# Kernel optimization log

Measured on AMD Instinct MI355X. Metric: run time of the kernel, lower is better.

The kernel has to match this reference:

```python
import math
import jax, jax.numpy as jnp
import numpy as np

B, T, FDIM, ODIM = 16, 16, 64, 8
NQ, LAYERS, DEGREE = 10, 2, 3
NA = 4                      # ceil(log2(T))
TOT = NQ + NA               # 14 total wires
NROTS = 4 * NQ * LAYERS     # 80 params per timestep
QROTS = 4 * NQ              # 40 (qff circuit, 1 layer)
C64 = jnp.complex64


def ry_mat(t):
    c = jnp.cos(0.5 * t).astype(C64)
    s = jnp.sin(0.5 * t).astype(C64)
    return jnp.stack([jnp.stack([c, -s], -1), jnp.stack([s, c], -1)], -2)


def rz_mat(t):
    p = jnp.exp(-0.5j * t.astype(C64))
    q = jnp.exp(0.5j * t.astype(C64))
    z = jnp.zeros_like(p)
    return jnp.stack([jnp.stack([p, z], -1), jnp.stack([z, q], -1)], -2)


def crx_mat(t):
    c = jnp.cos(0.5 * t).astype(C64)
    s = (-1j) * jnp.sin(0.5 * t).astype(C64)
    z = jnp.zeros_like(c)
    o = jnp.ones_like(c)
    r0 = jnp.stack([o, z, z, z], -1)
    r1 = jnp.stack([z, o, z, z], -1)
    r2 = jnp.stack([z, z, c, s], -1)
    r3 = jnp.stack([z, z, s, c], -1)
    return jnp.stack([r0, r1, r2, r3], -2)


CNOT = jnp.array([[1, 0, 0, 0], [0, 1, 0, 0], [0, 0, 0, 1], [0, 0, 1, 0]], dtype=C64)


def apply_gate(state, U, wires):
    # state: (Be, 2,...,2) tensor; wire w lives on axis w+1. U: (2^k,2^k) or (Be,2^k,2^k)
    k = len(wires)
    axes = [w + 1 for w in wires]
    st = jnp.moveaxis(state, axes, list(range(1, k + 1)))
    shp = st.shape
    st = st.reshape(shp[0], 2 ** k, -1)
    eq = 'bij,bjr->bir' if U.ndim == 3 else 'ij,bjr->bir'
    st = jnp.einsum(eq, U, st).reshape(shp)
    return jnp.moveaxis(st, list(range(1, k + 1)), axes)


def sim14_seq(nq, layers):
    # gate sequence of Sim et al. circuit 14: RY ring, CRX ring, RY ring, CRX counter-ring
    seq, idx = [], 0
    for _ in range(layers):
        for i in range(nq):
            seq.append(('ry', (i,), idx)); idx += 1
        for i in range(nq - 1, -1, -1):
            seq.append(('crx', (i, (i + 1) % nq), idx)); idx += 1
        for i in range(nq):
            seq.append(('ry', (i,), idx)); idx += 1
        for i in [nq - 1] + list(range(nq - 1)):
            seq.append(('crx', (i, (i - 1) % nq), idx)); idx += 1
    return seq


def apply_sim14(state, params, layers, adjoint=False):
    seq = sim14_seq(NQ, layers)
    if adjoint:
        seq = seq[::-1]
    sign = -1.0 if adjoint else 1.0
    for kind, w, pidx in seq:
        th = sign * params[..., pidx]
        U = ry_mat(th) if kind == 'ry' else crx_mat(th)
        state = apply_gate(state, U, list(w))
    return state


def apply_prepare(state, prep_p, adjoint=False):
    # learnable PREPARE ansatz on ancilla wires NQ..NQ+NA-1 (n_prep_layers == NA)
    seq = []
    for ly in range(NA):
        for qi in range(NA):
            seq.append(('ry', NQ + qi, (ly, qi, 0)))
            seq.append(('rz', NQ + qi, (ly, qi, 1)))
        for i in range(NA - 1):
            seq.append(('cnot', (NQ + i, NQ + i + 1), None))
    if adjoint:
        seq = seq[::-1]
    sign = -1.0 if adjoint else 1.0
    for kind, w, pix in seq:
        if kind == 'cnot':
            state = apply_gate(state, CNOT, list(w))
        else:
            th = sign * prep_p[pix]
            U = ry_mat(th) if kind == 'ry' else rz_mat(th)
            state = apply_gate(state, U, [w])
    return state


def pcphase(state, phi):
    # PennyLane PCPhase(phi, dim=2^NQ, wires=anc+main): e^{+i phi} on ancilla==0 subspace, e^{-i phi} elsewhere
    st = state.reshape(B, 2 ** NQ, 2 ** NA)
    ph = jnp.exp(1j * phi.astype(C64))
    vec = jnp.where(jnp.arange(2 ** NA) == 0, ph, jnp.conj(ph))
    return (st * vec).reshape((B,) + (2,) * TOT)


def apply_select(state, ts_params, adjoint=False):
    # Select: apply sim14(ts_params[:, j]) on main wires when ancilla register == j
    # (T == 2^NA so there is no identity padding). Vectorized over batch x ancilla index.
    st = state.reshape(B, 2 ** NQ, 2 ** NA)
    st = jnp.moveaxis(st, 2, 1).reshape((B * T,) + (2,) * NQ)
    st = apply_sim14(st, ts_params.reshape(B * T, NROTS), LAYERS, adjoint)
    st = st.reshape(B, 2 ** NA, 2 ** NQ)
    return jnp.moveaxis(st, 1, 2).reshape((B,) + (2,) * TOT)


def expvals(state):
    # <X_i>, <Y_i>, <Z_i> on main wires, order X0..X9, Y0..Y9, Z0..Z9
    xs, ys, zs = [], [], []
    for i in range(NQ):
        s = jnp.moveaxis(state, i + 1, 1).reshape(B, 2, -1)
        s0, s1 = s[:, 0], s[:, 1]
        c = jnp.sum(jnp.conj(s0) * s1, axis=-1)
        xs.append(2.0 * jnp.real(c))
        ys.append(2.0 * jnp.imag(c))
        zs.append(jnp.sum(jnp.abs(s0) ** 2 - jnp.abs(s1) ** 2, axis=-1))
    return jnp.stack(xs + ys + zs, axis=1).astype(jnp.float32)  # (B, 3*NQ)


def make_pe():
    pos = np.arange(T, dtype=np.float32)[:, None]
    div = np.exp(np.arange(0, FDIM, 2, dtype=np.float32) * -(math.log(10000.0) / FDIM))
    pe = np.zeros((T, FDIM), np.float32)
    pe[:, 0::2] = np.sin(pos * div)
    pe[:, 1::2] = np.cos(pos * div[:FDIM // 2])
    return jnp.asarray(pe)


def setup_inputs():
    key = jax.random.key(0)
    ks = jax.random.split(key, 8)
    return {
        'x': jax.random.normal(ks[0], (B, FDIM, T), jnp.float32),
        'W_fp': jax.random.normal(ks[1], (NROTS, FDIM), jnp.float32) / math.sqrt(FDIM),
        'b_fp': jnp.zeros((NROTS,), jnp.float32),
        'prep_p': 0.1 * jax.random.normal(ks[2], (NA, NA, 2), jnp.float32),
        'sig_ang': 0.1 * jax.random.normal(ks[3], (DEGREE + 1,), jnp.float32),
        'qff_p': jax.random.uniform(ks[4], (QROTS,), jnp.float32),
        'W_out': jax.random.normal(ks[5], (ODIM, 3 * NQ), jnp.float32) / math.sqrt(3 * NQ),
        'b_out': jnp.zeros((ODIM,), jnp.float32),
    }


def reference(x, W_fp, b_fp, prep_p, sig_ang, qff_p, W_out, b_out):
    h = jnp.transpose(x, (0, 2, 1)) + make_pe()[None]          # (B, T, FDIM)
    ts = jax.nn.sigmoid(h @ W_fp.T + b_fp) * (2.0 * math.pi)    # (B, T, NROTS)
    # |0...0> on all 14 wires, batched
    psi = jnp.zeros((B, 2 ** TOT), C64).at[:, 0].set(1.0).reshape((B,) + (2,) * TOT)
    psi = pcphase(psi, sig_ang[0])
    for k in range(DEGREE):
        psi = apply_prepare(psi, prep_p, adjoint=False)
        psi = apply_select(psi, ts, adjoint=(k % 2 == 1))
        psi = apply_prepare(psi, prep_p, adjoint=True)
        psi = pcphase(psi, sig_ang[k + 1])
    psi = apply_sim14(psi, qff_p, layers=1, adjoint=False)      # QFF readout circuit
    exps = expvals(psi)                                         # (B, 30)
    return exps @ W_out.T + b_out                               # (B, ODIM)
```

## Files before the change

kernel.cpp:

```cpp
#include <hip/hip_runtime.h>
#include <math.h>
#include <utility>


typedef float v2f __attribute__((ext_vector_type(2)));

struct Gate { int ry; int tbit; int cbit; int pidx; };
struct GateTab { Gate g[40]; };

constexpr GateTab make_gates1() {
  GateTab tb{};
  int pos = 0, idx = 0;
  for (int i = 0; i < 10; ++i) { tb.g[pos] = Gate{1, 9 - i, -1, idx}; ++pos; ++idx; }
  for (int i = 9; i >= 0; --i) { tb.g[pos] = Gate{0, 9 - ((i + 1) % 10), 9 - i, idx}; ++pos; ++idx; }
  for (int i = 0; i < 10; ++i) { tb.g[pos] = Gate{1, 9 - i, -1, idx}; ++pos; ++idx; }
  for (int k = 0; k < 10; ++k) {
    int i = (k == 0) ? 9 : (k - 1);
    tb.g[pos] = Gate{0, 9 - ((i + 9) % 10), 9 - i, idx}; ++pos; ++idx;
  }
  return tb;
}
constexpr GateTab GTC = make_gates1();

__device__ __forceinline__ int insert_zero(int v, int p) {
  return ((v >> p) << (p + 1)) | (v & ((1 << p) - 1));
}
__device__ __forceinline__ float2 cmul(float2 A, float2 B) {
  return make_float2(A.x * B.x - A.y * B.y, A.x * B.y + A.y * B.x);
}
__device__ __forceinline__ float2 conj2(float2 A) { return make_float2(A.x, -A.y); }
__device__ __forceinline__ v2f vmk(float x, float y) { v2f r; r.x = x; r.y = y; return r; }

template<int XM>
__device__ __forceinline__ float lxor(float v) {
  if constexpr (XM == 1) {
    int r = __builtin_amdgcn_update_dpp(__float_as_int(v), __float_as_int(v),
                                        0xB1, 0xF, 0xF, true);
    return __int_as_float(r);
  } else if constexpr (XM == 2) {
    int r = __builtin_amdgcn_update_dpp(__float_as_int(v), __float_as_int(v),
                                        0x4E, 0xF, 0xF, true);
    return __int_as_float(r);
  } else if constexpr (XM == 4) {
    int r = __builtin_amdgcn_ds_swizzle(__float_as_int(v), 0x101F);
    return __int_as_float(r);
  } else if constexpr (XM == 8) {
    int r = __builtin_amdgcn_update_dpp(__float_as_int(v), __float_as_int(v),
                                        0x128, 0xF, 0xF, true);
    return __int_as_float(r);
  } else if constexpr (XM == 16) {
#if __has_builtin(__builtin_amdgcn_permlane16_swap)
    unsigned uv = __float_as_uint(v);
    auto r = __builtin_amdgcn_permlane16_swap(uv, uv, false, false);
    return __uint_as_float(r[0] ^ r[1] ^ uv);
#else
    return __shfl_xor(v, 16, 64);
#endif
  } else {
#if __has_builtin(__builtin_amdgcn_permlane32_swap)
    unsigned uv = __float_as_uint(v);
    auto r = __builtin_amdgcn_permlane32_swap(uv, uv, false, false);
    return __uint_as_float(r[0] ^ r[1] ^ uv);
#else
    return __shfl_xor(v, 32, 64);
#endif
  }
}
template<int XM>
__device__ __forceinline__ v2f lxor2(v2f v) {
  v2f r; r.x = lxor<XM>(v.x); r.y = lxor<XM>(v.y); return r;
}

__device__ __forceinline__ float wave_sum(float v) {
  v += lxor<1>(v);
  v += lxor<2>(v);
  v += lxor<4>(v);
  v += lxor<8>(v);
  v += lxor<16>(v);
  v += lxor<32>(v);
  return v;
}

struct alignas(256) GBar {
  unsigned cnt;
  unsigned gen;
  unsigned done;
  unsigned pad[61];
};
__device__ GBar g_gb[16];

__device__ __forceinline__ void group_barrier16(int b, int lane) {
  unsigned snap = __hip_atomic_load(&g_gb[b].gen, __ATOMIC_RELAXED, __HIP_MEMORY_SCOPE_AGENT);
  if (lane == 0) {
    unsigned old = __hip_atomic_fetch_add(&g_gb[b].cnt, 1u, __ATOMIC_ACQ_REL,
                                          __HIP_MEMORY_SCOPE_AGENT);
    if ((old & 15u) == 15u)
      __hip_atomic_store(&g_gb[b].gen, snap + 1u, __ATOMIC_RELEASE,
                         __HIP_MEMORY_SCOPE_AGENT);
  }
  while (__hip_atomic_load(&g_gb[b].gen, __ATOMIC_RELAXED, __HIP_MEMORY_SCOPE_AGENT) == snap)
    __builtin_amdgcn_s_sleep(1);
  (void)__hip_atomic_load(&g_gb[b].gen, __ATOMIC_ACQUIRE, __HIP_MEMORY_SCOPE_AGENT);
}

template<int P>
__device__ __forceinline__ void ry_gate(v2f (&a)[16], float c, float s, int lane) {
  if constexpr (P < 4) {
    constexpr int m = 1 << P;
#pragma unroll
    for (int r0 = 0; r0 < 16; ++r0) {
      if (!(r0 & m)) {
        int r1 = r0 | m;
        v2f a0 = a[r0], a1 = a[r1];
        a[r0] = c * a0 - s * a1;
        a[r1] = s * a0 + c * a1;
      }
    }
  } else {
    constexpr int xm = 1 << (P - 4);
    bool up = (lane >> (P - 4)) & 1;
    float sg = up ? s : -s;
#pragma unroll
    for (int r = 0; r < 16; ++r) {
      v2f wv = lxor2<xm>(a[r]);
      a[r] = c * a[r] + sg * wv;
    }
  }
}

__device__ __forceinline__ v2f crot(v2f v, float c, float s, v2f w) {
  return c * v + s * vmk(w.y, -w.x);
}
template<int P>
__device__ __forceinline__ void crx_body(v2f (&a)[16], float c, float s, int lane) {
  if constexpr (P < 4) {
    constexpr int m = 1 << P;
#pragma unroll
    for (int r0 = 0; r0 < 16; ++r0) {
      if (!(r0 & m)) {
        int r1 = r0 | m;
        v2f a0 = a[r0], a1 = a[r1];
        a[r0] = crot(a0, c, s, a1);
        a[r1] = crot(a1, c, s, a0);
      }
    }
  } else {
    constexpr int xm = 1 << (P - 4);
#pragma unroll
    for (int r = 0; r < 16; ++r) {
      v2f wv = lxor2<xm>(a[r]);
      a[r] = crot(a[r], c, s, wv);
    }
  }
}

template<int P, int Q>
__device__ __forceinline__ void crx_gate(v2f (&a)[16], float c, float s, int lane) {
  if constexpr (Q >= 4) {
    bool act = (lane >> (Q - 4)) & 1;
    float cm = act ? c : 1.f;
    float sm = act ? s : 0.f;
    crx_body<P>(a, cm, sm, lane);
  } else {
    if constexpr (P < 4) {
      constexpr int m = 1 << P;
#pragma unroll
      for (int r0 = 0; r0 < 16; ++r0) {
        if (!(r0 & m) && ((r0 >> Q) & 1)) {
          int r1 = r0 | m;
          v2f a0 = a[r0], a1 = a[r1];
          a[r0] = crot(a0, c, s, a1);
          a[r1] = crot(a1, c, s, a0);
        }
      }
    } else {
      constexpr int xm = 1 << (P - 4);
#pragma unroll
      for (int r = 0; r < 16; ++r) {
        if ((r >> Q) & 1) {
          v2f wv = lxor2<xm>(a[r]);
          a[r] = crot(a[r], c, s, wv);
        }
      }
    }
  }
}

template<bool ADJ, int G>
__device__ __forceinline__ void one_gate(v2f (&a)[16], const float2* sc, int lane) {
  constexpr Gate g = GTC.g[ADJ ? (39 - G) : G];
  float2 scv = sc[g.pidx];
  float s = ADJ ? -scv.x : scv.x;
  float c = scv.y;
  if constexpr (g.ry != 0) ry_gate<g.tbit>(a, c, s, lane);
  else crx_gate<g.tbit, g.cbit>(a, c, s, lane);
}

template<bool ADJ, int... I>
__device__ __forceinline__ void run_layer_impl(v2f (&a)[16], const float2* sc,
                                               int lane, std::integer_sequence<int, I...>) {
  (one_gate<ADJ, I>(a, sc, lane), ...);
}
template<bool ADJ>
__device__ __forceinline__ void run_layer(v2f (&a)[16], const float2* sc, int lane) {
  run_layer_impl<ADJ>(a, sc, lane, std::make_integer_sequence<int, 40>{});
}

__global__ __launch_bounds__(256, 1) void k_fused(const float* __restrict__ x,
                                                  const float* __restrict__ W_fp,
                                                  const float* __restrict__ b_fp,
                                                  const float* __restrict__ prep,
                                                  const float* __restrict__ sig,
                                                  const float* __restrict__ qff,
                                                  const float* __restrict__ W_out,
                                                  const float* __restrict__ b_out,
                                                  float* __restrict__ out,
                                                  float4* __restrict__ part1,
                                                  float4* __restrict__ part2,
                                                  float* __restrict__ sv) {
  int blk = blockIdx.x;
  int b = blk & 15, sub = blk >> 4;
  int tid = threadIdx.x;
  int w = tid >> 6, lane = tid & 63;
  int aa = sub * 4 + w;

  __shared__ __align__(16) float h[4][64];
  __shared__ float2 scs[4][80];
  __shared__ float2 qscs[40];
  __shared__ float2 ps[32];
  __shared__ float2 es[4];
  __shared__ float2 u0s[16];
  __shared__ float4 R[2][512];

  if (sub == 0 && w == 0 && lane < 30) sv[b * 30 + lane] = 0.f;

  {
    int f = lane, k = f >> 1;
    float div = __expf(-(float)(2 * k) * (logf(10000.f) / 64.f));
    float ang = (float)aa * div;
    float sa, ca;
    __sincosf(ang, &sa, &ca);
    float pe = (f & 1) ? ca : sa;
    h[w][f] = x[(b * 64 + f) * 16 + aa] + pe;
  }
  if (w == 1) {
    if (lane < 32) {
      float s, cc;
      __sincosf(0.5f * prep[lane], &s, &cc);
      ps[lane] = make_float2(s, cc);
    } else if (lane < 36) {
      float s, cc;
      __sincosf(sig[lane - 32], &s, &cc);
      es[lane - 32] = make_float2(cc, s);
    }
  } else if (w == 2 && lane < 40) {
    float s, cc;
    __sincosf(0.5f * qff[lane], &s, &cc);
    qscs[lane] = make_float2(s, cc);
  }
  __syncthreads();

  if (w == 0) {
    float2 v[16];
#pragma unroll
    for (int i = 0; i < 16; ++i) v[i] = make_float2(i == 0 ? 1.f : 0.f, 0.f);
#pragma unroll 1
    for (int ly = 0; ly < 4; ++ly) {
#pragma unroll
      for (int qi = 0; qi < 4; ++qi) {
        int p = 3 - qi;
        float2 rc = ps[ly * 8 + qi * 2 + 0];
        {
          float s = rc.x, cc = rc.y;
#pragma unroll
          for (int m = 0; m < 8; ++m) {
            int a0 = insert_zero(m, p), a1 = a0 | (1 << p);
            float2 t0 = v[a0], t1 = v[a1];
            v[a0] = make_float2(cc * t0.x - s * t1.x, cc * t0.y - s * t1.y);
            v[a1] = make_float2(s * t0.x + cc * t1.x, s * t0.y + cc * t1.y);
          }
        }
        rc = ps[ly * 8 + qi * 2 + 1];
        {
          float s = rc.x, cc = rc.y;
#pragma unroll
          for (int m = 0; m < 8; ++m) {
            int a0 = insert_zero(m, p), a1 = a0 | (1 << p);
            float2 t0 = v[a0], t1 = v[a1];
            v[a0] = make_float2(cc * t0.x + s * t0.y, cc * t0.y - s * t0.x);
            v[a1] = make_float2(cc * t1.x - s * t1.y, cc * t1.y + s * t1.x);
          }
        }
      }
#pragma unroll
      for (int i = 0; i < 3; ++i) {
        int pc = 3 - i, pt = 2 - i;
#pragma unroll
        for (int m = 0; m < 4; ++m) {
          int mm = insert_zero(m, pt);
          mm = insert_zero(mm, pc);
          int a0 = mm | (1 << pc), a1 = a0 | (1 << pt);
          float2 t0 = v[a0], t1 = v[a1];
          v[a0] = t1; v[a1] = t0;
        }
      }
    }
    if (lane == 0) {
#pragma unroll
      for (int i = 0; i < 16; ++i) u0s[i] = v[i];
    }
  }

  {
    const float4* h4 = (const float4*)&h[w][0];
    for (int j = lane; j < 80; j += 64) {
      float acc = b_fp[j];
      const float4* w4 = (const float4*)(W_fp + j * 64);
#pragma unroll
      for (int k4 = 0; k4 < 16; ++k4) {
        float4 hh = h4[k4], ww = w4[k4];
        acc += hh.x * ww.x + hh.y * ww.y + hh.z * ww.z + hh.w * ww.w;
      }
      float sg = 1.f / (1.f + __expf(-acc));
      float s, cc;
      __sincosf(sg * 3.14159265358979323846f, &s, &cc);
      scs[w][j] = make_float2(s, cc);
    }
  }
  __syncthreads();

  float2 u0aa = u0s[aa];
  float2 e0 = es[0], e1 = es[1], e2 = es[2];
  float2 m0  = cmul(u0aa, e0);
  float2 cu0 = conj2(u0aa);
  float2 ceA = conj2(e1);
  float2 wA  = make_float2(-2.f * e1.y * u0aa.y, 2.f * e1.y * u0aa.x);
  float2 ceB = conj2(e2);
  float2 wB  = make_float2(-2.f * e2.y * u0aa.y, 2.f * e2.y * u0aa.x);

  const float2* sc = &scs[w][0];
  v2f a[16];
#pragma unroll
  for (int r = 0; r < 16; ++r) a[r] = vmk(0.f, 0.f);
  if (lane == 0) a[0] = vmk(m0.x, m0.y);

#pragma unroll 1
  for (int ph = 0; ph < 7; ++ph) {
    if (ph == 2 || ph == 4) {
      float2 ce = (ph == 2) ? ceA : ceB;
      float2 wk = (ph == 2) ? wA : wB;
      float4* part = (ph == 2) ? part1 : part2;

      __syncthreads();
      if (w < 2) {
#pragma unroll
        for (int q = 0; q < 8; ++q) {
          float2 p0 = cmul(cu0, make_float2(a[2 * q].x, a[2 * q].y));
          float2 p1 = cmul(cu0, make_float2(a[2 * q + 1].x, a[2 * q + 1].y));
          R[w][q * 64 + lane] = make_float4(p0.x, p0.y, p1.x, p1.y);
        }
      }
      __syncthreads();
      if (w >= 2) {
#pragma unroll
        for (int q = 0; q < 8; ++q) {
          float4 v = R[w - 2][q * 64 + lane];
          float2 p0 = cmul(cu0, make_float2(a[2 * q].x, a[2 * q].y));
          float2 p1 = cmul(cu0, make_float2(a[2 * q + 1].x, a[2 * q + 1].y));
          R[w - 2][q * 64 + lane] =
              make_float4(v.x + p0.x, v.y + p0.y, v.z + p1.x, v.w + p1.y);
        }
      }
      __syncthreads();
#pragma unroll
      for (int qq = 0; qq < 2; ++qq) {
        int q = w * 2 + qq;
        float4 v0 = R[0][q * 64 + lane];
        float4 v1 = R[1][q * 64 + lane];
        part[(size_t)(b * 4 + sub) * 512 + q * 64 + lane] =
            make_float4(v0.x + v1.x, v0.y + v1.y, v0.z + v1.z, v0.w + v1.w);
      }
      group_barrier16(b, lane);

      float4 s4[8];
#pragma unroll
      for (int q = 0; q < 8; ++q) {
        float4 v0 = R[0][q * 64 + lane];
        float4 v1 = R[1][q * 64 + lane];
        s4[q] = make_float4(v0.x + v1.x, v0.y + v1.y, v0.z + v1.z, v0.w + v1.w);
      }
#pragma unroll
      for (int o = 1; o < 4; ++o) {
        int so = (sub + o) & 3;
        const float4* pp = part + (size_t)(b * 4 + so) * 512 + lane;
#pragma unroll
        for (int q = 0; q < 8; ++q) {
          float4 v = pp[q * 64];
          s4[q].x += v.x; s4[q].y += v.y; s4[q].z += v.z; s4[q].w += v.w;
        }
      }
#pragma unroll
      for (int q = 0; q < 8; ++q) {
        v2f a0 = a[2 * q], a1 = a[2 * q + 1];
        a[2 * q] = vmk(ce.x * a0.x - ce.y * a0.y + wk.x * s4[q].x - wk.y * s4[q].y,
                       ce.x * a0.y + ce.y * a0.x + wk.x * s4[q].y + wk.y * s4[q].x);
        a[2 * q + 1] = vmk(ce.x * a1.x - ce.y * a1.y + wk.x * s4[q].z - wk.y * s4[q].w,
                           ce.x * a1.y + ce.y * a1.x + wk.x * s4[q].w + wk.y * s4[q].z);
      }
    }
    const float2* scp;
    if (ph == 6) scp = &qscs[0];
    else scp = sc + ((ph == 1 || ph == 2 || ph == 5) ? 40 : 0);
    if (ph == 2 || ph == 3) run_layer<true>(a, scp, lane);
    else                    run_layer<false>(a, scp, lane);
  }

  {
    float obs[30];
#pragma unroll
    for (int p = 0; p <= 9; ++p) {
      int i = 9 - p;
      float cr = 0.f, ci = 0.f, zz = 0.f;
      if (p < 4) {
        int m = 1 << p;
#pragma unroll
        for (int r0 = 0; r0 < 16; ++r0) {
          if (!(r0 & m)) {
            v2f A0 = a[r0], A1 = a[r0 | m];
            cr += A0.x * A1.x + A0.y * A1.y;
            ci += A0.x * A1.y - A0.y * A1.x;
            zz += (A0.x * A0.x + A0.y * A0.y) - (A1.x * A1.x + A1.y * A1.y);
          }
        }
      } else {
        int xm = 1 << (p - 4);
        bool up = (lane >> (p - 4)) & 1;
#pragma unroll
        for (int r = 0; r < 16; ++r) {
          float wx = __shfl_xor(a[r].x, xm, 64);
          float wy = __shfl_xor(a[r].y, xm, 64);
          float n2 = a[r].x * a[r].x + a[r].y * a[r].y;
          if (!up) {
            cr += a[r].x * wx + a[r].y * wy;
            ci += a[r].x * wy - a[r].y * wx;
            zz += n2;
          } else {
            zz -= n2;
          }
        }
      }
      obs[i] = 2.f * cr;
      obs[10 + i] = 2.f * ci;
      obs[20 + i] = zz;
    }
#pragma unroll
    for (int j = 0; j < 30; ++j) obs[j] = wave_sum(obs[j]);

    float* Rf = (float*)R;
    __syncthreads();
    if (lane == 0) {
#pragma unroll
      for (int j = 0; j < 30; ++j) Rf[w * 30 + j] = obs[j];
    }
    __syncthreads();
    if (w == 0) {
      if (lane < 30) {
        float v = Rf[0 * 30 + lane] + Rf[1 * 30 + lane] +
                  Rf[2 * 30 + lane] + Rf[3 * 30 + lane];
        atomicAdd(&sv[b * 30 + lane], v);
      }
      int lastflag = 0;
      if (lane == 0) {
        unsigned old = __hip_atomic_fetch_add(&g_gb[b].done, 1u, __ATOMIC_ACQ_REL,
                                              __HIP_MEMORY_SCOPE_AGENT);
        lastflag = ((old & 3u) == 3u) ? 1 : 0;
      }
      lastflag = __shfl(lastflag, 0, 64);
      if (lastflag) {
        (void)__hip_atomic_load(&g_gb[b].done, __ATOMIC_ACQUIRE, __HIP_MEMORY_SCOPE_AGENT);
        if (lane < 8) {
          float acc = b_out[lane];
#pragma unroll
          for (int j = 0; j < 30; ++j) acc += W_out[lane * 30 + j] * sv[b * 30 + j];
          out[b * 8 + lane] = acc;
        }
      }
    }
  }
}

extern "C" void kernel_launch(void* const* d_in, const int* in_sizes, int n_in,
                              void* d_out, int out_size, void* d_ws, size_t ws_size,
                              hipStream_t stream) {
  const float* x     = (const float*)d_in[0];
  const float* W_fp  = (const float*)d_in[1];
  const float* b_fp  = (const float*)d_in[2];
  const float* prep  = (const float*)d_in[3];
  const float* sig   = (const float*)d_in[4];
  const float* qff   = (const float*)d_in[5];
  const float* W_out = (const float*)d_in[6];
  const float* b_out = (const float*)d_in[7];
  float* out = (float*)d_out;
  (void)in_sizes; (void)n_in; (void)out_size;

  char* ws = (char*)d_ws;
  const size_t SZ_PART = (size_t)64 * 512 * 16;
  float4* part1 = (float4*)ws;
  float4* part2 = (float4*)(ws + SZ_PART);
  float*  sv    = (float*)(ws + 2 * SZ_PART);
  (void)ws_size;

  k_fused<<<dim3(64), dim3(256), 0, stream>>>(x, W_fp, b_fp, prep, sig, qff,
                                              W_out, b_out, out, part1, part2, sv);
}
```

Measured before the change: 159.2 us.

## Process two ancilla branches per wave and halve the grid with cheaper group barriers

Each wavefront now simulates two ancilla-index statevector slices (two sets of registers) instead of one, so the grid shrinks from 64 to 32 blocks and each batch group spans 2 blocks instead of 4. The cross-block barrier and partial-sum exchange now involve 8 waves and one peer block rather than 16 waves and three peers. The two independent slices also give each wave instruction-level parallelism to hide shuffle and arithmetic latency. In exchange, serial gate work per wave doubles, register pressure rises, and fewer CUs are used.

```diff
diff --git a/kernel.cpp b/kernel.cpp
--- a/kernel.cpp
+++ b/kernel.cpp
@@ -89,12 +89,12 @@
 };
 __device__ GBar g_gb[16];
 
-__device__ __forceinline__ void group_barrier16(int b, int lane) {
+__device__ __forceinline__ void group_barrier8(int b, int lane) {
   unsigned snap = __hip_atomic_load(&g_gb[b].gen, __ATOMIC_RELAXED, __HIP_MEMORY_SCOPE_AGENT);
   if (lane == 0) {
     unsigned old = __hip_atomic_fetch_add(&g_gb[b].cnt, 1u, __ATOMIC_ACQ_REL,
                                           __HIP_MEMORY_SCOPE_AGENT);
-    if ((old & 15u) == 15u)
+    if ((old & 7u) == 7u)
       __hip_atomic_store(&g_gb[b].gen, snap + 1u, __ATOMIC_RELEASE,
                          __HIP_MEMORY_SCOPE_AGENT);
   }
@@ -104,26 +104,35 @@
 }
 
 template<int P>
-__device__ __forceinline__ void ry_gate(v2f (&a)[16], float c, float s, int lane) {
+__device__ __forceinline__ void ry_gate(v2f (&a)[2][16], const float (&c)[2],
+                                        const float (&s)[2], int lane) {
   if constexpr (P < 4) {
     constexpr int m = 1 << P;
 #pragma unroll
-    for (int r0 = 0; r0 < 16; ++r0) {
-      if (!(r0 & m)) {
-        int r1 = r0 | m;
-        v2f a0 = a[r0], a1 = a[r1];
-        a[r0] = c * a0 - s * a1;
-        a[r1] = s * a0 + c * a1;
+    for (int q = 0; q < 2; ++q) {
+      float cc = c[q], ss = s[q];
+#pragma unroll
+      for (int r0 = 0; r0 < 16; ++r0) {
+        if (!(r0 & m)) {
+          int r1 = r0 | m;
+          v2f a0 = a[q][r0], a1 = a[q][r1];
+          a[q][r0] = cc * a0 - ss * a1;
+          a[q][r1] = ss * a0 + cc * a1;
+        }
       }
     }
   } else {
     constexpr int xm = 1 << (P - 4);
     bool up = (lane >> (P - 4)) & 1;
-    float sg = up ? s : -s;
-#pragma unroll
-    for (int r = 0; r < 16; ++r) {
-      v2f wv = lxor2<xm>(a[r]);
-      a[r] = c * a[r] + sg * wv;
+#pragma unroll
+    for (int q = 0; q < 2; ++q) {
+      float cc = c[q];
+      float sg = up ? s[q] : -s[q];
+#pragma unroll
+      for (int r = 0; r < 16; ++r) {
+        v2f wv = lxor2<xm>(a[q][r]);
+        a[q][r] = cc * a[q][r] + sg * wv;
+      }
     }
   }
 }
@@ -132,78 +141,100 @@
   return c * v + s * vmk(w.y, -w.x);
 }
 template<int P>
-__device__ __forceinline__ void crx_body(v2f (&a)[16], float c, float s, int lane) {
+__device__ __forceinline__ void crx_body(v2f (&a)[2][16], const float (&c)[2],
+                                         const float (&s)[2], int lane) {
   if constexpr (P < 4) {
     constexpr int m = 1 << P;
 #pragma unroll
-    for (int r0 = 0; r0 < 16; ++r0) {
-      if (!(r0 & m)) {
-        int r1 = r0 | m;
-        v2f a0 = a[r0], a1 = a[r1];
-        a[r0] = crot(a0, c, s, a1);
-        a[r1] = crot(a1, c, s, a0);
+    for (int q = 0; q < 2; ++q) {
+      float cc = c[q], ss = s[q];
+#pragma unroll
+      for (int r0 = 0; r0 < 16; ++r0) {
+        if (!(r0 & m)) {
+          int r1 = r0 | m;
+          v2f a0 = a[q][r0], a1 = a[q][r1];
+          a[q][r0] = crot(a0, cc, ss, a1);
+          a[q][r1] = crot(a1, cc, ss, a0);
+        }
       }
     }
   } else {
     constexpr int xm = 1 << (P - 4);
 #pragma unroll
-    for (int r = 0; r < 16; ++r) {
-      v2f wv = lxor2<xm>(a[r]);
-      a[r] = crot(a[r], c, s, wv);
+    for (int q = 0; q < 2; ++q) {
+      float cc = c[q], ss = s[q];
+#pragma unroll
+      for (int r = 0; r < 16; ++r) {
+        v2f wv = lxor2<xm>(a[q][r]);
+        a[q][r] = crot(a[q][r], cc, ss, wv);
+      }
     }
   }
 }
 
 template<int P, int Q>
-__device__ __forceinline__ void crx_gate(v2f (&a)[16], float c, float s, int lane) {
+__device__ __forceinline__ void crx_gate(v2f (&a)[2][16], const float (&c)[2],
+                                         const float (&s)[2], int lane) {
   if constexpr (Q >= 4) {
     bool act = (lane >> (Q - 4)) & 1;
-    float cm = act ? c : 1.f;
-    float sm = act ? s : 0.f;
+    float cm[2] = { act ? c[0] : 1.f, act ? c[1] : 1.f };
+    float sm[2] = { act ? s[0] : 0.f, act ? s[1] : 0.f };
     crx_body<P>(a, cm, sm, lane);
   } else {
     if constexpr (P < 4) {
       constexpr int m = 1 << P;
 #pragma unroll
-      for (int r0 = 0; r0 < 16; ++r0) {
-        if (!(r0 & m) && ((r0 >> Q) & 1)) {
-          int r1 = r0 | m;
-          v2f a0 = a[r0], a1 = a[r1];
-          a[r0] = crot(a0, c, s, a1);
-          a[r1] = crot(a1, c, s, a0);
+      for (int q = 0; q < 2; ++q) {
+        float cc = c[q], ss = s[q];
+#pragma unroll
+        for (int r0 = 0; r0 < 16; ++r0) {
+          if (!(r0 & m) && ((r0 >> Q) & 1)) {
+            int r1 = r0 | m;
+            v2f a0 = a[q][r0], a1 = a[q][r1];
+            a[q][r0] = crot(a0, cc, ss, a1);
+            a[q][r1] = crot(a1, cc, ss, a0);
+          }
         }
       }
     } else {
       constexpr int xm = 1 << (P - 4);
 #pragma unroll
-      for (int r = 0; r < 16; ++r) {
-        if ((r >> Q) & 1) {
-          v2f wv = lxor2<xm>(a[r]);
-          a[r] = crot(a[r], c, s, wv);
-        }
-      }
-    }
-  }
-}
-
-template<bool ADJ, int G>
-__device__ __forceinline__ void one_gate(v2f (&a)[16], const float2* sc, int lane) {
+      for (int q = 0; q < 2; ++q) {
+        float cc = c[q], ss = s[q];
+#pragma unroll
+        for (int r = 0; r < 16; ++r) {
+          if ((r >> Q) & 1) {
+            v2f wv = lxor2<xm>(a[q][r]);
+            a[q][r] = crot(a[q][r], cc, ss, wv);
+          }
+        }
+      }
+    }
+  }
+}
+
+template<bool ADJ, int CS, int G>
+__device__ __forceinline__ void one_gate(v2f (&a)[2][16], const float2* sc, int lane) {
   constexpr Gate g = GTC.g[ADJ ? (39 - G) : G];
-  float2 scv = sc[g.pidx];
-  float s = ADJ ? -scv.x : scv.x;
-  float c = scv.y;
+  float c[2], s[2];
+#pragma unroll
+  for (int q = 0; q < 2; ++q) {
+    float2 scv = sc[q * CS + g.pidx];
+    s[q] = ADJ ? -scv.x : scv.x;
+    c[q] = scv.y;
+  }
   if constexpr (g.ry != 0) ry_gate<g.tbit>(a, c, s, lane);
   else crx_gate<g.tbit, g.cbit>(a, c, s, lane);
 }
 
-template<bool ADJ, int... I>
-__device__ __forceinline__ void run_layer_impl(v2f (&a)[16], const float2* sc,
+template<bool ADJ, int CS, int... I>
+__device__ __forceinline__ void run_layer_impl(v2f (&a)[2][16], const float2* sc,
                                                int lane, std::integer_sequence<int, I...>) {
-  (one_gate<ADJ, I>(a, sc, lane), ...);
-}
-template<bool ADJ>
-__device__ __forceinline__ void run_layer(v2f (&a)[16], const float2* sc, int lane) {
-  run_layer_impl<ADJ>(a, sc, lane, std::make_integer_sequence<int, 40>{});
+  (one_gate<ADJ, CS, I>(a, sc, lane), ...);
+}
+template<bool ADJ, int CS>
+__device__ __forceinline__ void run_layer(v2f (&a)[2][16], const float2* sc, int lane) {
+  run_layer_impl<ADJ, CS>(a, sc, lane, std::make_integer_sequence<int, 40>{});
 }
 
 __global__ __launch_bounds__(256, 1) void k_fused(const float* __restrict__ x,
@@ -222,10 +253,11 @@
   int b = blk & 15, sub = blk >> 4;
   int tid = threadIdx.x;
   int w = tid >> 6, lane = tid & 63;
-  int aa = sub * 4 + w;
-
-  __shared__ __align__(16) float h[4][64];
-  __shared__ float2 scs[4][80];
+  int aa0 = sub * 8 + w * 2;
+  int aa1 = aa0 + 1;
+
+  __shared__ __align__(16) float h[8][64];
+  __shared__ float2 scs[8][80];
   __shared__ float2 qscs[40];
   __shared__ float2 ps[32];
   __shared__ float2 es[4];
@@ -234,14 +266,16 @@
 
   if (sub == 0 && w == 0 && lane < 30) sv[b * 30 + lane] = 0.f;
 
-  {
+#pragma unroll
+  for (int q = 0; q < 2; ++q) {
+    int cc = aa0 + q;
     int f = lane, k = f >> 1;
     float div = __expf(-(float)(2 * k) * (logf(10000.f) / 64.f));
-    float ang = (float)aa * div;
+    float ang = (float)cc * div;
     float sa, ca;
     __sincosf(ang, &sa, &ca);
     float pe = (f & 1) ? ca : sa;
-    h[w][f] = x[(b * 64 + f) * 16 + aa] + pe;
+    h[w * 2 + q][f] = x[(b * 64 + f) * 16 + cc] + pe;
   }
   if (w == 1) {
     if (lane < 32) {
@@ -311,8 +345,10 @@
     }
   }
 
-  {
-    const float4* h4 = (const float4*)&h[w][0];
+#pragma unroll 1
+  for (int q = 0; q < 2; ++q) {
+    int cc = w * 2 + q;
+    const float4* h4 = (const float4*)&h[cc][0];
     for (int j = lane; j < 80; j += 64) {
       float acc = b_fp[j];
       const float4* w4 = (const float4*)(W_fp + j * 64);
@@ -322,53 +358,67 @@
         acc += hh.x * ww.x + hh.y * ww.y + hh.z * ww.z + hh.w * ww.w;
       }
       float sg = 1.f / (1.f + __expf(-acc));
-      float s, cc;
-      __sincosf(sg * 3.14159265358979323846f, &s, &cc);
-      scs[w][j] = make_float2(s, cc);
+      float s, cf;
+      __sincosf(sg * 3.14159265358979323846f, &s, &cf);
+      scs[cc][j] = make_float2(s, cf);
     }
   }
   __syncthreads();
 
-  float2 u0aa = u0s[aa];
   float2 e0 = es[0], e1 = es[1], e2 = es[2];
-  float2 m0  = cmul(u0aa, e0);
-  float2 cu0 = conj2(u0aa);
-  float2 ceA = conj2(e1);
-  float2 wA  = make_float2(-2.f * e1.y * u0aa.y, 2.f * e1.y * u0aa.x);
-  float2 ceB = conj2(e2);
-  float2 wB  = make_float2(-2.f * e2.y * u0aa.y, 2.f * e2.y * u0aa.x);
-
-  const float2* sc = &scs[w][0];
-  v2f a[16];
-#pragma unroll
-  for (int r = 0; r < 16; ++r) a[r] = vmk(0.f, 0.f);
-  if (lane == 0) a[0] = vmk(m0.x, m0.y);
+  float2 u0c[2], m0c[2];
+  u0c[0] = u0s[aa0]; u0c[1] = u0s[aa1];
+  m0c[0] = cmul(u0c[0], e0); m0c[1] = cmul(u0c[1], e0);
+  float2 ceA = conj2(e1), ceB = conj2(e2);
+
+  const float2* sc = &scs[w * 2][0];
+  v2f a[2][16];
+#pragma unroll
+  for (int q = 0; q < 2; ++q) {
+#pragma unroll
+    for (int r = 0; r < 16; ++r) a[q][r] = vmk(0.f, 0.f);
+    if (lane == 0) a[q][0] = vmk(m0c[q].x, m0c[q].y);
+  }
 
 #pragma unroll 1
   for (int ph = 0; ph < 7; ++ph) {
     if (ph == 2 || ph == 4) {
       float2 ce = (ph == 2) ? ceA : ceB;
-      float2 wk = (ph == 2) ? wA : wB;
+      float ey = (ph == 2) ? e1.y : e2.y;
       float4* part = (ph == 2) ? part1 : part2;
 
       __syncthreads();
       if (w < 2) {
 #pragma unroll
-        for (int q = 0; q < 8; ++q) {
-          float2 p0 = cmul(cu0, make_float2(a[2 * q].x, a[2 * q].y));
-          float2 p1 = cmul(cu0, make_float2(a[2 * q + 1].x, a[2 * q + 1].y));
-          R[w][q * 64 + lane] = make_float4(p0.x, p0.y, p1.x, p1.y);
+        for (int qq = 0; qq < 8; ++qq) {
+          float px0 = 0.f, py0 = 0.f, px1 = 0.f, py1 = 0.f;
+#pragma unroll
+          for (int q = 0; q < 2; ++q) {
+            float2 cu = conj2(u0c[q]);
+            v2f a0 = a[q][2 * qq], a1 = a[q][2 * qq + 1];
+            px0 += cu.x * a0.x - cu.y * a0.y;
+            py0 += cu.x * a0.y + cu.y * a0.x;
+            px1 += cu.x * a1.x - cu.y * a1.y;
+            py1 += cu.x * a1.y + cu.y * a1.x;
+          }
+          R[w][qq * 64 + lane] = make_float4(px0, py0, px1, py1);
         }
       }
       __syncthreads();
       if (w >= 2) {
 #pragma unroll
-        for (int q = 0; q < 8; ++q) {
-          float4 v = R[w - 2][q * 64 + lane];
-          float2 p0 = cmul(cu0, make_float2(a[2 * q].x, a[2 * q].y));
-          float2 p1 = cmul(cu0, make_float2(a[2 * q + 1].x, a[2 * q + 1].y));
-          R[w - 2][q * 64 + lane] =
-              make_float4(v.x + p0.x, v.y + p0.y, v.z + p1.x, v.w + p1.y);
+        for (int qq = 0; qq < 8; ++qq) {
+          float4 v = R[w - 2][qq * 64 + lane];
+#pragma unroll
+          for (int q = 0; q < 2; ++q) {
+            float2 cu = conj2(u0c[q]);
+            v2f a0 = a[q][2 * qq], a1 = a[q][2 * qq + 1];
+            v.x += cu.x * a0.x - cu.y * a0.y;
+            v.y += cu.x * a0.y + cu.y * a0.x;
+            v.z += cu.x * a1.x - cu.y * a1.y;
+            v.w += cu.x * a1.y + cu.y * a1.x;
+          }
+          R[w - 2][qq * 64 + lane] = v;
         }
       }
       __syncthreads();
@@ -377,10 +427,10 @@
         int q = w * 2 + qq;
         float4 v0 = R[0][q * 64 + lane];
         float4 v1 = R[1][q * 64 + lane];
-        part[(size_t)(b * 4 + sub) * 512 + q * 64 + lane] =
+        part[(size_t)(b * 2 + sub) * 512 + q * 64 + lane] =
             make_float4(v0.x + v1.x, v0.y + v1.y, v0.z + v1.z, v0.w + v1.w);
       }
-      group_barrier16(b, lane);
+      group_barrier8(b, lane);
 
       float4 s4[8];
 #pragma unroll
@@ -389,10 +439,8 @@
         float4 v1 = R[1][q * 64 + lane];
         s4[q] = make_float4(v0.x + v1.x, v0.y + v1.y, v0.z + v1.z, v0.w + v1.w);
       }
-#pragma unroll
-      for (int o = 1; o < 4; ++o) {
-        int so = (sub + o) & 3;
-        const float4* pp = part + (size_t)(b * 4 + so) * 512 + lane;
+      {
+        const float4* pp = part + (size_t)(b * 2 + (sub ^ 1)) * 512 + lane;
 #pragma unroll
         for (int q = 0; q < 8; ++q) {
           float4 v = pp[q * 64];
@@ -400,19 +448,22 @@
         }
       }
 #pragma unroll
-      for (int q = 0; q < 8; ++q) {
-        v2f a0 = a[2 * q], a1 = a[2 * q + 1];
-        a[2 * q] = vmk(ce.x * a0.x - ce.y * a0.y + wk.x * s4[q].x - wk.y * s4[q].y,
-                       ce.x * a0.y + ce.y * a0.x + wk.x * s4[q].y + wk.y * s4[q].x);
-        a[2 * q + 1] = vmk(ce.x * a1.x - ce.y * a1.y + wk.x * s4[q].z - wk.y * s4[q].w,
-                           ce.x * a1.y + ce.y * a1.x + wk.x * s4[q].w + wk.y * s4[q].z);
-      }
-    }
-    const float2* scp;
-    if (ph == 6) scp = &qscs[0];
-    else scp = sc + ((ph == 1 || ph == 2 || ph == 5) ? 40 : 0);
-    if (ph == 2 || ph == 3) run_layer<true>(a, scp, lane);
-    else                    run_layer<false>(a, scp, lane);
+      for (int q = 0; q < 2; ++q) {
+        float2 wk = make_float2(-2.f * ey * u0c[q].y, 2.f * ey * u0c[q].x);
+#pragma unroll
+        for (int qq = 0; qq < 8; ++qq) {
+          v2f a0 = a[q][2 * qq], a1 = a[q][2 * qq + 1];
+          a[q][2 * qq] = vmk(ce.x * a0.x - ce.y * a0.y + wk.x * s4[qq].x - wk.y * s4[qq].y,
+                             ce.x * a0.y + ce.y * a0.x + wk.x * s4[qq].y + wk.y * s4[qq].x);
+          a[q][2 * qq + 1] = vmk(ce.x * a1.x - ce.y * a1.y + wk.x * s4[qq].z - wk.y * s4[qq].w,
+                                 ce.x * a1.y + ce.y * a1.x + wk.x * s4[qq].w + wk.y * s4[qq].z);
+        }
+      }
+    }
+    if (ph == 2)      run_layer<true, 80>(a, sc + 40, lane);
+    else if (ph == 3) run_layer<true, 80>(a, sc, lane);
+    else if (ph == 6) run_layer<false, 0>(a, &qscs[0], lane);
+    else              run_layer<false, 80>(a, sc + ((ph == 1 || ph == 5) ? 40 : 0), lane);
   }
 
   {
@@ -424,28 +475,34 @@
       if (p < 4) {
         int m = 1 << p;
 #pragma unroll
-        for (int r0 = 0; r0 < 16; ++r0) {
-          if (!(r0 & m)) {
-            v2f A0 = a[r0], A1 = a[r0 | m];
-            cr += A0.x * A1.x + A0.y * A1.y;
-            ci += A0.x * A1.y - A0.y * A1.x;
-            zz += (A0.x * A0.x + A0.y * A0.y) - (A1.x * A1.x + A1.y * A1.y);
+        for (int q = 0; q < 2; ++q) {
+#pragma unroll
+          for (int r0 = 0; r0 < 16; ++r0) {
+            if (!(r0 & m)) {
+              v2f A0 = a[q][r0], A1 = a[q][r0 | m];
+              cr += A0.x * A1.x + A0.y * A1.y;
+              ci += A0.x * A1.y - A0.y * A1.x;
+              zz += (A0.x * A0.x + A0.y * A0.y) - (A1.x * A1.x + A1.y * A1.y);
+            }
           }
         }
       } else {
         int xm = 1 << (p - 4);
         bool up = (lane >> (p - 4)) & 1;
 #pragma unroll
-        for (int r = 0; r < 16; ++r) {
-          float wx = __shfl_xor(a[r].x, xm, 64);
-          float wy = __shfl_xor(a[r].y, xm, 64);
-          float n2 = a[r].x * a[r].x + a[r].y * a[r].y;
-          if (!up) {
-            cr += a[r].x * wx + a[r].y * wy;
-            ci += a[r].x * wy - a[r].y * wx;
-            zz += n2;
-          } else {
-            zz -= n2;
+        for (int q = 0; q < 2; ++q) {
+#pragma unroll
+          for (int r = 0; r < 16; ++r) {
+            float wx = __shfl_xor(a[q][r].x, xm, 64);
+            float wy = __shfl_xor(a[q][r].y, xm, 64);
+            float n2 = a[q][r].x * a[q][r].x + a[q][r].y * a[q][r].y;
+            if (!up) {
+              cr += a[q][r].x * wx + a[q][r].y * wy;
+              ci += a[q][r].x * wy - a[q][r].y * wx;
+              zz += n2;
+            } else {
+              zz -= n2;
+            }
           }
         }
       }
@@ -473,7 +530,7 @@
       if (lane == 0) {
         unsigned old = __hip_atomic_fetch_add(&g_gb[b].done, 1u, __ATOMIC_ACQ_REL,
                                               __HIP_MEMORY_SCOPE_AGENT);
-        lastflag = ((old & 3u) == 3u) ? 1 : 0;
+        lastflag = ((old & 1u) == 1u) ? 1 : 0;
       }
       lastflag = __shfl(lastflag, 0, 64);
       if (lastflag) {
@@ -504,12 +561,12 @@
   (void)in_sizes; (void)n_in; (void)out_size;
 
   char* ws = (char*)d_ws;
-  const size_t SZ_PART = (size_t)64 * 512 * 16;
+  const size_t SZ_PART = (size_t)32 * 512 * 16;
   float4* part1 = (float4*)ws;
   float4* part2 = (float4*)(ws + SZ_PART);
   float*  sv    = (float*)(ws + 2 * SZ_PART);
   (void)ws_size;
 
-  k_fused<<<dim3(64), dim3(256), 0, stream>>>(x, W_fp, b_fp, prep, sig, qff,
+  k_fused<<<dim3(32), dim3(256), 0, stream>>>(x, W_fp, b_fp, prep, sig, qff,
                                               W_out, b_out, out, part1, part2, sv);
 }
```

After: 219.4 us. 1.38x slower.
